# Performance work log

Hardware: AMD Instinct MI355X
Metric: run time of the kernel (lower is better)

Reference implementation:

```python
import jax, jax.numpy as jnp
import numpy as np

D, H, T, P1, P2, B = 1024, 16, 2048, 16, 16, 2
HD = D // H
EPS = 1e-6
NEG = -1e30


def _ln(x, g, b):
    mu = jnp.mean(x, axis=-1, keepdims=True)
    var = jnp.mean((x - mu) ** 2, axis=-1, keepdims=True)
    return (x - mu) * jax.lax.rsqrt(var + EPS) * g + b


def _split_heads(x):  # [B,S,D] -> [B,H,S,HD]
    b, s, _ = x.shape
    return x.reshape(b, s, H, HD).transpose(0, 2, 1, 3)


def _merge_heads(x):  # [B,H,S,HD] -> [B,S,D]
    b, _, s, _ = x.shape
    return x.transpose(0, 2, 1, 3).reshape(b, s, D)


def setup_inputs() -> dict:
    key = jax.random.key(0)
    ks = jax.random.split(key, 24)
    s = 0.02
    inp = {
        'x': jax.random.normal(ks[0], (B, T, D), jnp.float32),
        'p1': jax.random.normal(ks[1], (B, P1, D), jnp.float32),
        'p2': jax.random.normal(ks[2], (B, P2, D), jnp.float32),
        'prior_1': jax.random.uniform(ks[3], (B, T), jnp.float32),
        'prior_2': jax.random.uniform(ks[4], (B, T), jnp.float32),
        'mask': jnp.ones((B, T), jnp.float32),
        'Wq': s * jax.random.normal(ks[5], (D, D), jnp.float32),
        'bq': jnp.zeros((D,), jnp.float32),
        'Wk': s * jax.random.normal(ks[6], (D, D), jnp.float32),
        'bk': jnp.zeros((D,), jnp.float32),
        'Wv': s * jax.random.normal(ks[7], (D, D), jnp.float32),
        'bv': jnp.zeros((D,), jnp.float32),
        'ln2_g': jnp.ones((D,), jnp.float32),
        'ln2_b': jnp.zeros((D,), jnp.float32),
        'W1': s * jax.random.normal(ks[8], (D, D), jnp.float32),
        'b1': jnp.zeros((D,), jnp.float32),
        'W2': s * jax.random.normal(ks[9], (D, D), jnp.float32),
        'b2': jnp.zeros((D,), jnp.float32),
        'Wp1': s * jax.random.normal(ks[10], (D, D), jnp.float32),
        'bp1': jnp.zeros((D,), jnp.float32),
        'Wp2': s * jax.random.normal(ks[11], (D, D), jnp.float32),
        'bp2': jnp.zeros((D,), jnp.float32),
    }
    return inp


def reference(x, p1, p2, prior_1, prior_2, mask, Wq, bq, Wk, bk, Wv, bv,
              ln2_g, ln2_b, W1, b1, W2, b2, Wp1, bp1, Wp2, bp2):
    scale = 1.0 / jnp.sqrt(jnp.asarray(HD, x.dtype))
    # Q/K are [proj(x); p1; p2] (prompts enter unprojected), V only from x.
    q = _split_heads(jnp.concatenate([x @ Wq + bq, p1, p2], axis=1))
    k = _split_heads(jnp.concatenate([x @ Wk + bk, p1, p2], axis=1))
    v = _split_heads(x @ Wv + bv)
    scores = jnp.einsum('bhqd,bhkd->bhqk', q, k) * scale  # [B,H,T+P,T+P]

    word = scores[:, :, :T, :T]                                  # [B,H,T,T]
    p1s = jnp.swapaxes(scores[:, :, :T, T:T + P1], -1, -2)       # [B,H,P1,T]
    p2s = jnp.swapaxes(scores[:, :, :T, T + P1:], -1, -2)        # [B,H,P2,T]

    word = word + (1.0 - mask)[:, None, None, :] * NEG           # mask_logits
    wa = jax.nn.softmax(word, axis=-1)
    p1a = jax.nn.softmax(jax.nn.softmax(p1s, axis=-1) * prior_1[:, None, None, :], axis=-1)
    p2a = jax.nn.softmax(jax.nn.softmax(p2s, axis=-1) * prior_2[:, None, None, :], axis=-1)

    ctx = jnp.einsum('bhqk,bhkd->bhqd', wa, v)    # [B,H,T,HD]
    p1_v = jnp.einsum('bhpk,bhkd->bhpd', p1a, ctx)
    p2_v = jnp.einsum('bhpk,bhkd->bhpd', p2a, ctx)

    residual = x + _merge_heads(ctx)
    out = _ln(residual, ln2_g, ln2_b)
    out = jax.nn.gelu(out @ W1 + b1, approximate=False)
    out = out @ W2 + b2 + residual

    p1_out = _ln(_merge_heads(p1_v) + p1, ln2_g, ln2_b)
    p1_out = jax.nn.gelu(p1_out @ Wp1 + bp1, approximate=False)

    p2_out = _ln(_merge_heads(p2_v) + p2, ln2_g, ln2_b)
    p2_out = jax.nn.gelu(p2_out @ Wp2 + bp2, approximate=False)
    return (out, p1_out, p2_out)
```

## Files before the change

### kernel.cpp

```cpp
#include <hip/hip_runtime.h>

#define DEV __device__ __forceinline__

typedef unsigned short u16;
typedef unsigned int   u32;
typedef short  s16x8  __attribute__((ext_vector_type(8)));
typedef float  f32x4  __attribute__((ext_vector_type(4)));
typedef float  f32x16 __attribute__((ext_vector_type(16)));

constexpr int Bc = 2, Hc = 16, Tc = 2048, Dc = 1024, HDc = 64, Mc = 4096;
constexpr int TP = Tc + 32;
constexpr float SCALEc = 0.125f;
constexpr float LOG2E = 1.44269504088896340736f;
constexpr float SCALE2c = SCALEc * LOG2E;
constexpr float NEGc = -1e30f;

typedef __attribute__((address_space(3))) void lds_void;
typedef const __attribute__((address_space(1))) void g_void;

DEV void gload16(const void* g, void* l) {
  __builtin_amdgcn_global_load_lds((g_void*)g, (lds_void*)l, 16, 0, 0);
}

DEV int swz(int r) { return (r & 7) ^ ((r >> 3) & 7); }

DEV u32 bfr(float f) {
  u32 u = __float_as_uint(f);
  return (u + 0x7fffu + ((u >> 16) & 1u)) >> 16;
}
DEV u32 cvtpk(float a, float b) {
  u32 r;
  asm("v_cvt_pk_bf16_f32 %0, %1, %2" : "=v"(r) : "v"(a), "v"(b));
  return r;
}
DEV s16x8 mk8(u32 w0, u32 w1, u32 w2, u32 w3) {
  union { u32 u[4]; s16x8 v; } x;
  x.u[0] = w0; x.u[1] = w1; x.u[2] = w2; x.u[3] = w3;
  return x.v;
}
DEV float geluf(float x) { return 0.5f * x * (1.0f + erff(x * 0.70710678118654752440f)); }

DEV float wredS(float v) {
  #pragma unroll
  for (int o = 32; o; o >>= 1) v += __shfl_xor(v, o);
  return v;
}
DEV float wredM(float v) {
  #pragma unroll
  for (int o = 32; o; o >>= 1) v = fmaxf(v, __shfl_xor(v, o));
  return v;
}
DEV float bredS(float v, float* sm) {
  v = wredS(v);
  __syncthreads();
  if ((threadIdx.x & 63) == 0) sm[threadIdx.x >> 6] = v;
  __syncthreads();
  return sm[0] + sm[1] + sm[2] + sm[3];
}
DEV float bredM(float v, float* sm) {
  v = wredM(v);
  __syncthreads();
  if ((threadIdx.x & 63) == 0) sm[threadIdx.x >> 6] = v;
  __syncthreads();
  return fmaxf(fmaxf(sm[0], sm[1]), fmaxf(sm[2], sm[3]));
}

__global__ __launch_bounds__(256) void transpose_w5_k(
    const float* __restrict__ Wq, const float* __restrict__ Wk,
    const float* __restrict__ Wv, const float* __restrict__ W1,
    const float* __restrict__ W2, const float* __restrict__ x,
    u16* __restrict__ WQKVT, u16* __restrict__ W1T, u16* __restrict__ W2T,
    u16* __restrict__ XB) {
  int z = blockIdx.z;
  if (z == 5) {
    int base = (int)(blockIdx.y * 32 + blockIdx.x);
    int i0 = base * 1024 + (int)threadIdx.x;
    #pragma unroll
    for (int k = 0; k < 4; ++k) {
      int i = i0 + k * 256;
      float4 v = ((const float4*)x)[i];
      ushort4 u;
      u.x = (u16)bfr(v.x); u.y = (u16)bfr(v.y);
      u.z = (u16)bfr(v.z); u.w = (u16)bfr(v.w);
      ((ushort4*)XB)[i] = u;
    }
    return;
  }
  __shared__ float tile[32][33];
  int bx = blockIdx.x, by = blockIdx.y;
  const float* src = (z == 0) ? Wq : (z == 1) ? Wk : (z == 2) ? Wv
                    : (z == 3) ? W1 : W2;
  u16* dst = (z == 0) ? WQKVT
           : (z == 1) ? WQKVT + (size_t)1024 * 1024
           : (z == 2) ? WQKVT + (size_t)2 * 1024 * 1024
           : (z == 3) ? W1T : W2T;
  int tx = threadIdx.x & 31, ty = threadIdx.x >> 5;
  #pragma unroll
  for (int i = 0; i < 32; i += 8)
    tile[ty + i][tx] = src[(size_t)(by * 32 + ty + i) * Dc + bx * 32 + tx];
  __syncthreads();
  #pragma unroll
  for (int i = 0; i < 32; i += 8)
    dst[(size_t)(bx * 32 + ty + i) * Dc + by * 32 + tx] = (u16)bfr(tile[tx][ty + i]);
}

template <int MODE, int NBX, int NBY>
__global__ __launch_bounds__(256, 3) void gemm128_k(
    const u16* __restrict__ A, const u16* __restrict__ Bt,
    const float* __restrict__ bias0, const float* __restrict__ bias1,
    const float* __restrict__ bias2,
    u16* __restrict__ outQ, u16* __restrict__ outK, u16* __restrict__ outVT,
    u16* __restrict__ outB, float* __restrict__ outF,
    const float* __restrict__ resid) {
  __shared__ __align__(16) u16 smem[17408];
  u16* as0 = smem;
  u16* bs0 = smem + 2 * 128 * 32;
  const int tid = threadIdx.x, lane = tid & 63, wave = tid >> 6;
  const int wr = wave >> 1, wc = wave & 1;
  constexpr int RPX = NBX / 4, CPX = NBY / 2;
  const int bid = (int)blockIdx.x;
  const int xcd = bid & 7, l = bid >> 3;
  const int row0 = ((xcd & 3) * RPX + l % RPX) * 128;
  const int col0 = ((xcd >> 2) * CPX + l / RPX) * 128;

  f32x4 zero4;
  #pragma unroll
  for (int r = 0; r < 4; ++r) zero4[r] = 0.f;
  f32x4 acc[4][4];
  #pragma unroll
  for (int i = 0; i < 4; ++i)
    #pragma unroll
    for (int j = 0; j < 4; ++j) acc[i][j] = zero4;

  auto stage = [&](int buf, int kt) {
    const int k0 = kt * 32;
    #pragma unroll
    for (int is = 0; is < 2; ++is) {
      int q = is * 256 + tid; int r = q >> 2, c = q & 3, g = c ^ ((r >> 1) & 3);
      gload16(A + (size_t)(row0 + r) * Dc + k0 + g * 8,
              as0 + (size_t)buf * 4096 + (is * 256 + wave * 64) * 8);
    }
    #pragma unroll
    for (int is = 0; is < 2; ++is) {
      int q = is * 256 + tid; int r = q >> 2, c = q & 3, g = c ^ ((r >> 1) & 3);
      gload16(Bt + (size_t)(col0 + r) * Dc + k0 + g * 8,
              bs0 + (size_t)buf * 4096 + (is * 256 + wave * 64) * 8);
    }
  };

  stage(0, 0);
  asm volatile("s_waitcnt vmcnt(0)" ::: "memory");
  __syncthreads();

  int cur = 0;
  for (int kt = 0; kt < 32; ++kt) {
    if (kt + 1 < 32) stage(cur ^ 1, kt + 1);
    s16x8 af[4], bfv[4];
    #pragma unroll
    for (int f = 0; f < 4; ++f) {
      int r = wr * 64 + f * 16 + (lane & 15);
      int c = (lane >> 4) ^ ((r >> 1) & 3);
      af[f] = *(const s16x8*)&as0[cur * 4096 + r * 32 + c * 8];
    }
    #pragma unroll
    for (int f = 0; f < 4; ++f) {
      int r = wc * 64 + f * 16 + (lane & 15);
      int c = (lane >> 4) ^ ((r >> 1) & 3);
      bfv[f] = *(const s16x8*)&bs0[cur * 4096 + r * 32 + c * 8];
    }
    __builtin_amdgcn_s_setprio(1);
    #pragma unroll
    for (int i = 0; i < 4; ++i)
      #pragma unroll
      for (int j = 0; j < 4; ++j)
        acc[i][j] = __builtin_amdgcn_mfma_f32_16x16x32_bf16(af[i], bfv[j], acc[i][j], 0, 0, 0);
    __builtin_amdgcn_s_setprio(0);
    __syncthreads();
    cur ^= 1;
  }

  if (MODE == 0) {
    const int which = col0 >> 10;
    const float* bias = (which == 0) ? bias0 : (which == 1) ? bias1 : bias2;
    if (which == 2) {
      const int CSV = 129;
      u16* ct = smem;
      #pragma unroll
      for (int i = 0; i < 4; ++i)
        #pragma unroll
        for (int j = 0; j < 4; ++j)
          #pragma unroll
          for (int r = 0; r < 4; ++r) {
            int rl = wr * 64 + i * 16 + (lane >> 4) * 4 + r;
            int cl = wc * 64 + j * 16 + (lane & 15);
            float v = acc[i][j][r] + bias[(col0 + cl) & 1023];
            ct[rl * CSV + cl] = (u16)bfr(v);
          }
      __syncthreads();
      int bb = row0 >> 11, tbase = row0 & 2047;
      #pragma unroll
      for (int it = 0; it < 16; ++it) {
        int linear = it * 256 + tid;
        int dcol = linear >> 5, q4 = linear & 31;
        int t = q4 * 4;
        int n = (col0 & 1023) + dcol;
        int hh = n >> 6, dd = n & 63;
        ushort4 val;
        val.x = ct[(t + 0) * CSV + dcol];
        val.y = ct[(t + 1) * CSV + dcol];
        val.z = ct[(t + 2) * CSV + dcol];
        val.w = ct[(t + 3) * CSV + dcol];
        *(ushort4*)&outVT[((size_t)(bb * Hc + hh) * 64 + dd) * Tc + tbase + t] = val;
      }
    } else {
      const int CS = 136;
      u16* ct = smem;
      #pragma unroll
      for (int i = 0; i < 4; ++i)
        #pragma unroll
        for (int j = 0; j < 4; ++j)
          #pragma unroll
          for (int r = 0; r < 4; ++r) {
            int rl = wr * 64 + i * 16 + (lane >> 4) * 4 + r;
            int cl = wc * 64 + j * 16 + (lane & 15);
            float v = acc[i][j][r] + bias[(col0 + cl) & 1023];
            ct[rl * CS + cl] = (u16)bfr(v);
          }
      __syncthreads();
      #pragma unroll
      for (int it = 0; it < 16; ++it) {
        int linear = it * 256 + tid;
        int row = linear >> 5, c4 = (linear & 31) * 4;
        ushort4 val = *(const ushort4*)&ct[row * CS + c4];
        int grow = row0 + row;
        int col = col0 + c4;
        int n = col & 1023;
        int hh = n >> 6, d = n & 63, bb = grow >> 11, t = grow & 2047;
        if (which == 0)
          *(ushort4*)&outQ[(((size_t)(bb * Hc + hh) * Tc + t) << 6) + d] = val;
        else
          *(ushort4*)&outK[(((size_t)(bb * Hc + hh) * TP + t) << 6) + d] = val;
      }
    }
  } else if (MODE == 1) {
    const int CS = 136;
    u16* ct = smem;
    #pragma unroll
    for (int i = 0; i < 4; ++i)
      #pragma unroll
      for (int j = 0; j < 4; ++j)
        #pragma unroll
        for (int r = 0; r < 4; ++r) {
          int rl = wr * 64 + i * 16 + (lane >> 4) * 4 + r;
          int cl = wc * 64 + j * 16 + (lane & 15);
          float v = geluf(acc[i][j][r] + bias0[col0 + cl]);
          ct[rl * CS + cl] = (u16)bfr(v);
        }
    __syncthreads();
    #pragma unroll
    for (int it = 0; it < 16; ++it) {
      int linear = it * 256 + tid;
      int row = linear >> 5, c4 = (linear & 31) * 4;
      ushort4 val = *(const ushort4*)&ct[row * CS + c4];
      *(ushort4*)&outB[(size_t)(row0 + row) * Dc + col0 + c4] = val;
    }
  } else {
    const int CSF = 132;
    float* cf = (float*)smem;
    #pragma unroll
    for (int p = 0; p < 2; ++p) {
      if (wr == p) {
        #pragma unroll
        for (int i = 0; i < 4; ++i)
          #pragma unroll
          for (int j = 0; j < 4; ++j)
            #pragma unroll
            for (int r = 0; r < 4; ++r) {
              int rl = i * 16 + (lane >> 4) * 4 + r;
              int cl = wc * 64 + j * 16 + (lane & 15);
              cf[rl * CSF + cl] = acc[i][j][r];
            }
      }
      __syncthreads();
      #pragma unroll
      for (int it = 0; it < 8; ++it) {
        int linear = it * 256 + tid;
        int row = linear >> 5, c4 = (linear & 31) * 4;
        float4 v = *(const float4*)&cf[row * CSF + c4];
        int grow = row0 + p * 64 + row;
        int col = col0 + c4;
        float4 rr = *(const float4*)&resid[(size_t)grow * Dc + col];
        float4 o;
        o.x = v.x + bias0[col + 0] + rr.x;
        o.y = v.y + bias0[col + 1] + rr.y;
        o.z = v.z + bias0[col + 2] + rr.z;
        o.w = v.w + bias0[col + 3] + rr.w;
        *(float4*)&outF[(size_t)grow * Dc + col] = o;
      }
      __syncthreads();
    }
  }
}

__global__ __launch_bounds__(256, 2) void attn_k(
    const u16* __restrict__ qb,
    const u16* __restrict__ kb,
    const u16* __restrict__ vt,
    const float* __restrict__ maskp,
    const float* __restrict__ p1, const float* __restrict__ p2,
    float* __restrict__ OP0, float* __restrict__ OP1,
    float* __restrict__ ML,
    float* __restrict__ SP) {
  __shared__ __align__(16) u16 kls[2][64 * 64];
  __shared__ __align__(16) u16 vls[2][64 * 64];
  __shared__ __align__(16) u16 kpls[32 * 64];
  __shared__ float mls[1024];

  const int tid = threadIdx.x, lane = tid & 63, wave = tid >> 6;
  const int wg = ((int)blockIdx.x & 7) * 128 + ((int)blockIdx.x >> 3);
  const int ks = wg & 1, qt = (wg >> 1) & 15, bh = wg >> 5;
  const int b = bh >> 4;
  const int lo = lane & 31, h5 = lane >> 5;
  const size_t kbase = (size_t)bh * TP * 64;
  const size_t vbase = (size_t)bh * 64 * Tc;

  for (int i = tid; i < 1024; i += 256)
    mls[i] = (1.0f - maskp[(size_t)b * Tc + ks * 1024 + i]) * NEGc;

  if (ks == 0) {
    int r = tid >> 3, cg = tid & 7, g = cg ^ swz(r);
    int h = bh & 15;
    const float* src = (r < 16)
        ? (p1 + (size_t)(b * 16 + r) * Dc + h * 64 + g * 8)
        : (p2 + (size_t)(b * 16 + (r - 16)) * Dc + h * 64 + g * 8);
    float4 a = *(const float4*)src;
    float4 c = *(const float4*)(src + 4);
    *(s16x8*)&kpls[tid * 8] = mk8(cvtpk(a.x, a.y), cvtpk(a.z, a.w),
                                  cvtpk(c.x, c.y), cvtpk(c.z, c.w));
  }

  const int q0 = qt * 128 + wave * 32;
  s16x8 qf[4];
  #pragma unroll
  for (int kc = 0; kc < 4; ++kc)
    qf[kc] = *(const s16x8*)(qb + ((size_t)bh * Tc + q0 + lo) * 64 + kc * 16 + h5 * 8);

  auto stageKV = [&](int buf, int kt2) {
    #pragma unroll
    for (int is = 0; is < 2; ++is) {
      int q = is * 256 + tid; int r = q >> 3, c = q & 7, g = c ^ swz(r);
      gload16(kb + kbase + (size_t)(kt2 * 64 + r) * 64 + g * 8,
              &kls[buf][(is * 256 + wave * 64) * 8]);
      gload16(vt + vbase + (size_t)r * Tc + kt2 * 64 + g * 8,
              &vls[buf][(is * 256 + wave * 64) * 8]);
    }
  };

  stageKV(0, ks * 16);
  asm volatile("s_waitcnt vmcnt(0)" ::: "memory");
  __syncthreads();

  f32x16 zero16;
  #pragma unroll
  for (int r = 0; r < 16; ++r) zero16[r] = 0.f;
  f32x16 O0 = zero16, O1 = zero16, racc = zero16;

  int cur = 0;
  for (int kt = 0; kt < 16; ++kt) {
    if (kt + 1 < 16) stageKV(cur ^ 1, ks * 16 + kt + 1);

    #pragma unroll
    for (int c = 0; c < 2; ++c) {
      f32x16 s = zero16;
      __builtin_amdgcn_s_setprio(1);
      #pragma unroll
      for (int kc = 0; kc < 4; ++kc) {
        int r = c * 32 + lo;
        int ci = (kc * 2 + h5) ^ swz(r);
        s16x8 kf = *(const s16x8*)&kls[cur][r * 64 + ci * 8];
        s = __builtin_amdgcn_mfma_f32_32x32x16_bf16(kf, qf[kc], s, 0, 0, 0);
      }
      __builtin_amdgcn_s_setprio(0);

      float4 mq[4];
      #pragma unroll
      for (int g = 0; g < 4; ++g)
        mq[g] = *(const float4*)&mls[kt * 64 + c * 32 + 4 * h5 + 8 * g];

      float p[16];
      #pragma unroll
      for (int r = 0; r < 16; ++r) {
        float mv = (&mq[r >> 2].x)[r & 3];
        p[r] = exp2f(s[r] * SCALE2c + mv);
        racc[r] += p[r];
      }

      #pragma unroll
      for (int k1 = 0; k1 < 2; ++k1) {
        u32 w0 = cvtpk(p[8 * k1 + 0], p[8 * k1 + 1]);
        u32 w1 = cvtpk(p[8 * k1 + 2], p[8 * k1 + 3]);
        u32 w2 = cvtpk(p[8 * k1 + 4], p[8 * k1 + 5]);
        u32 w3 = cvtpk(p[8 * k1 + 6], p[8 * k1 + 7]);
        asm volatile("v_permlane32_swap_b32 %0, %1" : "+v"(w2), "+v"(w0));
        asm volatile("v_permlane32_swap_b32 %0, %1" : "+v"(w3), "+v"(w1));
        s16x8 pf = mk8(w0, w1, w2, w3);
        __builtin_amdgcn_s_setprio(1);
        #pragma unroll
        for (int db = 0; db < 2; ++db) {
          int d = db * 32 + lo;
          int ci = (c * 4 + k1 * 2 + h5) ^ swz(d);
          s16x8 vf = *(const s16x8*)&vls[cur][d * 64 + ci * 8];
          if (db == 0) O0 = __builtin_amdgcn_mfma_f32_32x32x16_bf16(pf, vf, O0, 0, 0, 0);
          else         O1 = __builtin_amdgcn_mfma_f32_32x32x16_bf16(pf, vf, O1, 0, 0, 0);
        }
        __builtin_amdgcn_s_setprio(0);
      }
    }
    __syncthreads();
    cur ^= 1;
  }

  if (ks == 0) {
    f32x16 sp = zero16;
    #pragma unroll
    for (int kc = 0; kc < 4; ++kc) {
      int ci = (kc * 2 + h5) ^ swz(lo);
      s16x8 kf = *(const s16x8*)&kpls[lo * 64 + ci * 8];
      sp = __builtin_amdgcn_mfma_f32_32x32x16_bf16(kf, qf[kc], sp, 0, 0, 0);
    }
    #pragma unroll
    for (int r = 0; r < 16; ++r) {
      int pr = (r & 3) + 8 * (r >> 2) + 4 * h5;
      SP[((size_t)bh * 32 + pr) * Tc + q0 + lo] = sp[r] * SCALEc;
    }
  }

  float* dst = ks ? OP1 : OP0;
  #pragma unroll
  for (int r = 0; r < 16; ++r) {
    int row = q0 + (r & 3) + 8 * (r >> 2) + 4 * h5;
    dst[((size_t)bh * Tc + row) * 64 + lo]      = O0[r];
    dst[((size_t)bh * Tc + row) * 64 + 32 + lo] = O1[r];
  }
  float lt = 0.f;
  #pragma unroll
  for (int r = 0; r < 16; ++r) lt += racc[r];
  lt += __shfl_xor(lt, 32);
  if (lane < 32)
    ML[((size_t)ks * 32 + bh) * Tc + q0 + lo] = lt;
}

__global__ __launch_bounds__(256) void prompt_softmax_k(float* __restrict__ SP,
                                                        const float* __restrict__ pr1,
                                                        const float* __restrict__ pr2) {
  __shared__ float sm[4];
  int row = blockIdx.x;
  int bh = row >> 5, p = row & 31, b = bh >> 4;
  const float* prior = (p < 16 ? pr1 : pr2) + (size_t)b * Tc;
  float* s = SP + (size_t)row * Tc;
  int tid = threadIdx.x;
  float v[8], pw[8];
  #pragma unroll
  for (int i = 0; i < 8; ++i) { int t = tid + i * 256; v[i] = s[t]; pw[i] = prior[t]; }
  float mx = -INFINITY;
  #pragma unroll
  for (int i = 0; i < 8; ++i) mx = fmaxf(mx, v[i]);
  mx = bredM(mx, sm);
  float sum = 0.f;
  #pragma unroll
  for (int i = 0; i < 8; ++i) { v[i] = __expf(v[i] - mx); sum += v[i]; }
  sum = bredS(sum, sm);
  float inv = 1.0f / sum;
  float mx2 = -INFINITY;
  #pragma unroll
  for (int i = 0; i < 8; ++i) { v[i] = v[i] * inv * pw[i]; mx2 = fmaxf(mx2, v[i]); }
  mx2 = bredM(mx2, sm);
  float sum2 = 0.f;
  #pragma unroll
  for (int i = 0; i < 8; ++i) { v[i] = __expf(v[i] - mx2); sum2 += v[i]; }
  sum2 = bredS(sum2, sm);
  float inv2 = 1.0f / sum2;
  #pragma unroll
  for (int i = 0; i < 8; ++i) s[tid + i * 256] = v[i] * inv2;
}

__global__ __launch_bounds__(256) void pv_partial_k(const float* __restrict__ PA,
                                                    float* __restrict__ ctx,
                                                    const float* __restrict__ OP1,
                                                    const float* __restrict__ ML,
                                                    float* __restrict__ PVP) {
  __shared__ float pal[32][128];
  __shared__ float lsm[128];
  const int bh = blockIdx.x, ts = blockIdx.y;
  const int tid = threadIdx.x;
  const int t0 = ts * 128;
  const float* pabase = PA + (size_t)bh * 32 * Tc;

  if (tid < 128) {
    size_t r = (size_t)bh * Tc + t0 + tid;
    lsm[tid] = 1.0f / (ML[r] + ML[(size_t)32 * Tc + r]);
  }
  __syncthreads();
  #pragma unroll
  for (int pp = 0; pp < 8; ++pp) {
    int idx = pp * 256 + tid;
    int rr = idx >> 4, c4 = (idx & 15) * 4;
    size_t row = (size_t)bh * Tc + t0 + rr;
    float4 v0 = *(const float4*)(ctx + row * 64 + c4);
    float4 v1 = *(const float4*)(OP1 + row * 64 + c4);
    float li = lsm[rr];
    float4 o;
    o.x = (v0.x + v1.x) * li;
    o.y = (v0.y + v1.y) * li;
    o.z = (v0.z + v1.z) * li;
    o.w = (v0.w + v1.w) * li;
    *(float4*)(ctx + row * 64 + c4) = o;
  }
  __syncthreads();

  #pragma unroll
  for (int i = 0; i < 4; ++i) {
    int e = tid + i * 256;
    int p = e >> 5, c4 = e & 31;
    *(float4*)&pal[p][c4 * 4] = *(const float4*)&pabase[(size_t)p * Tc + t0 + c4 * 4];
  }
  __syncthreads();

  const int d4 = tid & 15, p0 = tid >> 4;
  const float* cb = ctx + ((size_t)bh * Tc + t0) * 64 + d4 * 4;
  float4 a0 = make_float4(0.f, 0.f, 0.f, 0.f);
  float4 a1 = make_float4(0.f, 0.f, 0.f, 0.f);
  for (int tt = 0; tt < 128; ++tt) {
    float4 v = *(const float4*)(cb + (size_t)tt * 64);
    float w0 = pal[p0][tt], w1 = pal[p0 + 16][tt];
    a0.x += w0 * v.x; a0.y += w0 * v.y; a0.z += w0 * v.z; a0.w += w0 * v.w;
    a1.x += w1 * v.x; a1.y += w1 * v.y; a1.z += w1 * v.z; a1.w += w1 * v.w;
  }
  float* o = PVP + (((size_t)ts * 32 + bh) * 32) * 64 + d4 * 4;
  *(float4*)(o + (size_t)p0 * 64) = a0;
  *(float4*)(o + (size_t)(p0 + 16) * 64) = a1;
}

__global__ __launch_bounds__(256) void resln_k(const float* __restrict__ x,
                                               const float* __restrict__ ctx,
                                               const float* __restrict__ g,
                                               const float* __restrict__ be,
                                               float* __restrict__ res,
                                               u16* __restrict__ lnout) {
  __shared__ float sm[4];
  int row = blockIdx.x;
  int b = row >> 11, t = row & 2047;
  int tid = threadIdx.x, c4 = tid * 4;
  int h = c4 >> 6, d = c4 & 63;
  float4 xv = *(const float4*)(x + (size_t)row * Dc + c4);
  float4 cv = *(const float4*)(ctx + (((size_t)(b * Hc + h) * Tc + t) << 6) + d);
  float r0 = xv.x + cv.x, r1 = xv.y + cv.y, r2 = xv.z + cv.z, r3 = xv.w + cv.w;
  float4 rr; rr.x = r0; rr.y = r1; rr.z = r2; rr.w = r3;
  *(float4*)(res + (size_t)row * Dc + c4) = rr;
  float s = bredS(r0 + r1 + r2 + r3, sm);
  float sq = bredS(r0 * r0 + r1 * r1 + r2 * r2 + r3 * r3, sm);
  float mu = s * (1.0f / Dc);
  float var = sq * (1.0f / Dc) - mu * mu;
  float rs = rsqrtf(var + 1e-6f);
  ushort4 o;
  o.x = (u16)bfr((r0 - mu) * rs * g[c4 + 0] + be[c4 + 0]);
  o.y = (u16)bfr((r1 - mu) * rs * g[c4 + 1] + be[c4 + 1]);
  o.z = (u16)bfr((r2 - mu) * rs * g[c4 + 2] + be[c4 + 2]);
  o.w = (u16)bfr((r3 - mu) * rs * g[c4 + 3] + be[c4 + 3]);
  *(ushort4*)(lnout + (size_t)row * Dc + c4) = o;
}

__global__ __launch_bounds__(256) void promptln_k(const float* __restrict__ PVP,
                                                  const float* __restrict__ p1,
                                                  const float* __restrict__ p2,
                                                  const float* __restrict__ g,
                                                  const float* __restrict__ be,
                                                  float* __restrict__ PMLN) {
  __shared__ float sm[4];
  int row = blockIdx.x;
  int b = row >> 5, j = row & 31;
  int tid = threadIdx.x, c4 = tid * 4;
  int h = c4 >> 6, d = c4 & 63;
  int bh = b * Hc + h;
  const float* pr = (j < 16) ? (p1 + (size_t)(b * 16 + j) * Dc + c4)
                             : (p2 + (size_t)(b * 16 + j - 16) * Dc + c4);
  float4 pv4 = make_float4(0.f, 0.f, 0.f, 0.f);
  #pragma unroll
  for (int ts = 0; ts < 16; ++ts) {
    float4 v = *(const float4*)(PVP + (((size_t)ts * 32 + bh) * 32 + j) * 64 + d);
    pv4.x += v.x; pv4.y += v.y; pv4.z += v.z; pv4.w += v.w;
  }
  float4 pp4 = *(const float4*)pr;
  float r0 = pv4.x + pp4.x, r1 = pv4.y + pp4.y, r2 = pv4.z + pp4.z, r3 = pv4.w + pp4.w;
  float s = bredS(r0 + r1 + r2 + r3, sm);
  float sq = bredS(r0 * r0 + r1 * r1 + r2 * r2 + r3 * r3, sm);
  float mu = s * (1.0f / Dc);
  float var = sq * (1.0f / Dc) - mu * mu;
  float rs = rsqrtf(var + 1e-6f);
  float4 o;
  o.x = (r0 - mu) * rs * g[c4 + 0] + be[c4 + 0];
  o.y = (r1 - mu) * rs * g[c4 + 1] + be[c4 + 1];
  o.z = (r2 - mu) * rs * g[c4 + 2] + be[c4 + 2];
  o.w = (r3 - mu) * rs * g[c4 + 3] + be[c4 + 3];
  *(float4*)(PMLN + (size_t)row * Dc + c4) = o;
}

__global__ __launch_bounds__(256) void pffn_partial_k(const float* __restrict__ PMLN,
                                                      const float* __restrict__ Wp1,
                                                      const float* __restrict__ Wp2,
                                                      float* __restrict__ PB) {
  __shared__ float pm[32][32];
  const int tid = threadIdx.x;
  const int ks = blockIdx.x, ct = blockIdx.y, s = blockIdx.z;
  const int c = ct * 256 + tid;
  const int k0 = ks * 32;
  const float* W = s ? Wp2 : Wp1;

  #pragma unroll
  for (int i = 0; i < 4; ++i) {
    int e = tid + i * 256;
    int r = e >> 5, kk = e & 31;
    int grow = (r >> 4) * 32 + s * 16 + (r & 15);
    pm[r][kk] = PMLN[(size_t)grow * Dc + k0 + kk];
  }
  __syncthreads();

  float acc[32];
  #pragma unroll
  for (int r = 0; r < 32; ++r) acc[r] = 0.f;
  for (int kk = 0; kk < 32; ++kk) {
    float w = W[(size_t)(k0 + kk) * Dc + c];
    #pragma unroll
    for (int r = 0; r < 32; ++r) acc[r] += pm[r][kk] * w;
  }

  float* pb = PB + (((size_t)ks * 2 + s) * 32) * Dc + c;
  #pragma unroll
  for (int r = 0; r < 32; ++r) pb[(size_t)r * Dc] = acc[r];
}

__global__ __launch_bounds__(256) void pffn_reduce_k(const float* __restrict__ PB,
                                                     const float* __restrict__ bp1,
                                                     const float* __restrict__ bp2,
                                                     float* __restrict__ out) {
  int e = blockIdx.x * 256 + threadIdx.x;
  int s = e >> 15, rem = e & 32767;
  int r = rem >> 10, c = rem & 1023;
  float sum = 0.f;
  const float* pb = PB + ((size_t)s * 32 + r) * Dc + c;
  #pragma unroll
  for (int ks = 0; ks < 32; ++ks) sum += pb[(size_t)ks * 2 * 32 * Dc];
  const float* bp = s ? bp2 : bp1;
  out[(size_t)Mc * Dc + (size_t)s * (32 * Dc) + (size_t)r * Dc + c] = geluf(sum + bp[c]);
}

extern "C" void kernel_launch(void* const* d_in, const int* in_sizes, int n_in,
                              void* d_out, int out_size, void* d_ws, size_t ws_size,
                              hipStream_t stream) {
  (void)in_sizes; (void)n_in; (void)out_size; (void)ws_size;
  const float* x   = (const float*)d_in[0];
  const float* p1  = (const float*)d_in[1];
  const float* p2  = (const float*)d_in[2];
  const float* pr1 = (const float*)d_in[3];
  const float* pr2 = (const float*)d_in[4];
  const float* msk = (const float*)d_in[5];
  const float* Wq  = (const float*)d_in[6];
  const float* bq  = (const float*)d_in[7];
  const float* Wk  = (const float*)d_in[8];
  const float* bk  = (const float*)d_in[9];
  const float* Wv  = (const float*)d_in[10];
  const float* bv  = (const float*)d_in[11];
  const float* g2  = (const float*)d_in[12];
  const float* be2 = (const float*)d_in[13];
  const float* W1  = (const float*)d_in[14];
  const float* b1  = (const float*)d_in[15];
  const float* W2  = (const float*)d_in[16];
  const float* b2  = (const float*)d_in[17];
  const float* Wp1 = (const float*)d_in[18];
  const float* bp1 = (const float*)d_in[19];
  const float* Wp2 = (const float*)d_in[20];
  const float* bp2 = (const float*)d_in[21];

  char* ws = (char*)d_ws;
  size_t off = 0;
  auto alloc = [&](size_t bytes) {
    void* p = ws + off;
    off += (bytes + 255) & ~(size_t)255;
    return p;
  };
  u16* WQKVT = (u16*)alloc((size_t)3072 * 1024 * 2);
  u16* W1T   = (u16*)alloc((size_t)1024 * 1024 * 2);
  u16* W2T   = (u16*)alloc((size_t)1024 * 1024 * 2);
  u16* XB    = (u16*)alloc((size_t)Mc * Dc * 2);
  u16* QB    = (u16*)alloc((size_t)32 * Tc * 64 * 2);
  u16* KB    = (u16*)alloc((size_t)32 * TP * 64 * 2);
  u16* H1    = (u16*)alloc((size_t)Mc * Dc * 2);
  u16* VT    = (u16*)alloc((size_t)32 * 64 * Tc * 2);
  float* CTX = (float*)alloc((size_t)32 * Tc * 64 * 4);
  float* SP  = (float*)alloc((size_t)32 * 32 * Tc * 4);
  float* RES = (float*)alloc((size_t)Mc * Dc * 4);
  float* PMLN = (float*)alloc((size_t)64 * Dc * 4);
  float* ML  = (float*)alloc((size_t)2 * 32 * Tc * 4);
  float* PVP = (float*)alloc((size_t)16 * 32 * 32 * 64 * 4);
  u16* LNOUT = XB;
  float* PB  = SP;
  float* OP0 = CTX;
  float* OP1 = RES;

  float* outMain = (float*)d_out;

  transpose_w5_k<<<dim3(32, 32, 6), 256, 0, stream>>>(Wq, Wk, Wv, W1, W2, x,
                                                      WQKVT, W1T, W2T, XB);
  gemm128_k<0, 32, 24><<<768, 256, 0, stream>>>(XB, WQKVT, bq, bk, bv, QB, KB,
                                                VT, nullptr, nullptr, nullptr);
  attn_k<<<1024, 256, 0, stream>>>(QB, KB, VT, msk, p1, p2, OP0, OP1, ML, SP);
  prompt_softmax_k<<<1024, 256, 0, stream>>>(SP, pr1, pr2);
  pv_partial_k<<<dim3(32, 16), 256, 0, stream>>>(SP, OP0, OP1, ML, PVP);
  resln_k<<<4096, 256, 0, stream>>>(x, CTX, g2, be2, RES, LNOUT);
  promptln_k<<<64, 256, 0, stream>>>(PVP, p1, p2, g2, be2, PMLN);
  pffn_partial_k<<<dim3(32, 4, 2), 256, 0, stream>>>(PMLN, Wp1, Wp2, PB);
  pffn_reduce_k<<<256, 256, 0, stream>>>(PB, bp1, bp2, outMain);
  gemm128_k<1, 32, 8><<<256, 256, 0, stream>>>(LNOUT, W1T, b1, nullptr, nullptr,
                                               nullptr, nullptr, nullptr, H1,
                                               nullptr, nullptr);
  gemm128_k<2, 32, 8><<<256, 256, 0, stream>>>(H1, W2T, b2, nullptr, nullptr,
                                               nullptr, nullptr, nullptr, nullptr,
                                               outMain, RES);
}
```

Baseline: 211.7 us.

## Store attention partial outputs as bf16 and widen the transpose tiles

```diff
diff --git a/kernel.cpp b/kernel.cpp
--- a/kernel.cpp
+++ b/kernel.cpp
@@ -28,6 +28,7 @@
   u32 u = __float_as_uint(f);
   return (u + 0x7fffu + ((u >> 16) & 1u)) >> 16;
 }
+DEV float b2f(u32 lo16) { return __uint_as_float(lo16 << 16); }
 DEV u32 cvtpk(float a, float b) {
   u32 r;
   asm("v_cvt_pk_bf16_f32 %0, %1, %2" : "=v"(r) : "v"(a), "v"(b));
@@ -73,10 +74,10 @@
     u16* __restrict__ XB) {
   int z = blockIdx.z;
   if (z == 5) {
-    int base = (int)(blockIdx.y * 32 + blockIdx.x);
-    int i0 = base * 1024 + (int)threadIdx.x;
-    #pragma unroll
-    for (int k = 0; k < 4; ++k) {
+    int base = (int)(blockIdx.y * 16 + blockIdx.x);
+    int i0 = base * 4096 + (int)threadIdx.x;
+    #pragma unroll
+    for (int k = 0; k < 16; ++k) {
       int i = i0 + k * 256;
       float4 v = ((const float4*)x)[i];
       ushort4 u;
@@ -86,7 +87,7 @@
     }
     return;
   }
-  __shared__ float tile[32][33];
+  __shared__ float tile[64][65];
   int bx = blockIdx.x, by = blockIdx.y;
   const float* src = (z == 0) ? Wq : (z == 1) ? Wk : (z == 2) ? Wv
                     : (z == 3) ? W1 : W2;
@@ -94,14 +95,22 @@
            : (z == 1) ? WQKVT + (size_t)1024 * 1024
            : (z == 2) ? WQKVT + (size_t)2 * 1024 * 1024
            : (z == 3) ? W1T : W2T;
-  int tx = threadIdx.x & 31, ty = threadIdx.x >> 5;
-  #pragma unroll
-  for (int i = 0; i < 32; i += 8)
-    tile[ty + i][tx] = src[(size_t)(by * 32 + ty + i) * Dc + bx * 32 + tx];
-  __syncthreads();
-  #pragma unroll
-  for (int i = 0; i < 32; i += 8)
-    dst[(size_t)(bx * 32 + ty + i) * Dc + by * 32 + tx] = (u16)bfr(tile[tx][ty + i]);
+  int tx = threadIdx.x & 63, ty = threadIdx.x >> 6;
+  #pragma unroll
+  for (int i = 0; i < 64; i += 4)
+    tile[ty + i][tx] = src[(size_t)(by * 64 + ty + i) * Dc + bx * 64 + tx];
+  __syncthreads();
+  int quad = threadIdx.x & 15, rw0 = threadIdx.x >> 4;
+  #pragma unroll
+  for (int it = 0; it < 4; ++it) {
+    int rw = it * 16 + rw0;
+    ushort4 u;
+    u.x = (u16)bfr(tile[quad * 4 + 0][rw]);
+    u.y = (u16)bfr(tile[quad * 4 + 1][rw]);
+    u.z = (u16)bfr(tile[quad * 4 + 2][rw]);
+    u.w = (u16)bfr(tile[quad * 4 + 3][rw]);
+    *(ushort4*)&dst[(size_t)(bx * 64 + rw) * Dc + by * 64 + quad * 4] = u;
+  }
 }
 
 template <int MODE, int NBX, int NBY>
@@ -308,7 +317,7 @@
     const u16* __restrict__ vt,
     const float* __restrict__ maskp,
     const float* __restrict__ p1, const float* __restrict__ p2,
-    float* __restrict__ OP0, float* __restrict__ OP1,
+    u16* __restrict__ OP0B, u16* __restrict__ OP1B,
     float* __restrict__ ML,
     float* __restrict__ SP) {
   __shared__ __align__(16) u16 kls[2][64 * 64];
@@ -435,12 +444,17 @@
     }
   }
 
-  float* dst = ks ? OP1 : OP0;
+  u32* dstw = (u32*)(ks ? OP1B : OP0B);
   #pragma unroll
   for (int r = 0; r < 16; ++r) {
     int row = q0 + (r & 3) + 8 * (r >> 2) + 4 * h5;
-    dst[((size_t)bh * Tc + row) * 64 + lo]      = O0[r];
-    dst[((size_t)bh * Tc + row) * 64 + 32 + lo] = O1[r];
+    int srcE = (h5 << 5) | ((2 * lo) & 31);
+    int srcO = (h5 << 5) | ((2 * lo + 1) & 31);
+    float aE = __shfl(O0[r], srcE), bE = __shfl(O1[r], srcE);
+    float aO = __shfl(O0[r], srcO), bO = __shfl(O1[r], srcO);
+    float vE = (lo < 16) ? aE : bE;
+    float vO = (lo < 16) ? aO : bO;
+    dstw[((size_t)bh * Tc + row) * 32 + lo] = cvtpk(vE, vO);
   }
   float lt = 0.f;
   #pragma unroll
@@ -485,9 +499,10 @@
 }
 
 __global__ __launch_bounds__(256) void pv_partial_k(const float* __restrict__ PA,
+                                                    const u16* __restrict__ OP0B,
+                                                    const u16* __restrict__ OP1B,
+                                                    const float* __restrict__ ML,
                                                     float* __restrict__ ctx,
-                                                    const float* __restrict__ OP1,
-                                                    const float* __restrict__ ML,
                                                     float* __restrict__ PVP) {
   __shared__ float pal[32][128];
   __shared__ float lsm[128];
@@ -495,6 +510,8 @@
   const int tid = threadIdx.x;
   const int t0 = ts * 128;
   const float* pabase = PA + (size_t)bh * 32 * Tc;
+  const u32* w0p = (const u32*)OP0B;
+  const u32* w1p = (const u32*)OP1B;
 
   if (tid < 128) {
     size_t r = (size_t)bh * Tc + t0 + tid;
@@ -505,16 +522,16 @@
   for (int pp = 0; pp < 8; ++pp) {
     int idx = pp * 256 + tid;
     int rr = idx >> 4, c4 = (idx & 15) * 4;
-    size_t row = (size_t)bh * Tc + t0 + rr;
-    float4 v0 = *(const float4*)(ctx + row * 64 + c4);
-    float4 v1 = *(const float4*)(OP1 + row * 64 + c4);
+    size_t rowb = ((size_t)bh * Tc + t0 + rr) * 32 + (c4 >> 1);
+    u32 a0 = w0p[rowb], a1 = w0p[rowb + 1];
+    u32 b0 = w1p[rowb], b1 = w1p[rowb + 1];
     float li = lsm[rr];
     float4 o;
-    o.x = (v0.x + v1.x) * li;
-    o.y = (v0.y + v1.y) * li;
-    o.z = (v0.z + v1.z) * li;
-    o.w = (v0.w + v1.w) * li;
-    *(float4*)(ctx + row * 64 + c4) = o;
+    o.x = (b2f(a0 & 0xffffu) + b2f(b0 & 0xffffu)) * li;
+    o.y = (b2f(a0 >> 16)     + b2f(b0 >> 16))     * li;
+    o.z = (b2f(a1 & 0xffffu) + b2f(b1 & 0xffffu)) * li;
+    o.w = (b2f(a1 >> 16)     + b2f(b1 >> 16))     * li;
+    *(float4*)(ctx + ((size_t)bh * Tc + t0 + rr) * 64 + c4) = o;
   }
   __syncthreads();
 
@@ -704,18 +721,18 @@
   float* PVP = (float*)alloc((size_t)16 * 32 * 32 * 64 * 4);
   u16* LNOUT = XB;
   float* PB  = SP;
-  float* OP0 = CTX;
-  float* OP1 = RES;
+  u16* OP0B  = (u16*)RES;
+  u16* OP1B  = (u16*)RES + (size_t)32 * Tc * 64;
 
   float* outMain = (float*)d_out;
 
-  transpose_w5_k<<<dim3(32, 32, 6), 256, 0, stream>>>(Wq, Wk, Wv, W1, W2, x,
+  transpose_w5_k<<<dim3(16, 16, 6), 256, 0, stream>>>(Wq, Wk, Wv, W1, W2, x,
                                                       WQKVT, W1T, W2T, XB);
   gemm128_k<0, 32, 24><<<768, 256, 0, stream>>>(XB, WQKVT, bq, bk, bv, QB, KB,
                                                 VT, nullptr, nullptr, nullptr);
-  attn_k<<<1024, 256, 0, stream>>>(QB, KB, VT, msk, p1, p2, OP0, OP1, ML, SP);
+  attn_k<<<1024, 256, 0, stream>>>(QB, KB, VT, msk, p1, p2, OP0B, OP1B, ML, SP);
   prompt_softmax_k<<<1024, 256, 0, stream>>>(SP, pr1, pr2);
-  pv_partial_k<<<dim3(32, 16), 256, 0, stream>>>(SP, OP0, OP1, ML, PVP);
+  pv_partial_k<<<dim3(32, 16), 256, 0, stream>>>(SP, OP0B, OP1B, ML, CTX, PVP);
   resln_k<<<4096, 256, 0, stream>>>(x, CTX, g2, be2, RES, LNOUT);
   promptln_k<<<64, 256, 0, stream>>>(PVP, p1, p2, g2, be2, PMLN);
   pffn_partial_k<<<dim3(32, 4, 2), 256, 0, stream>>>(PMLN, Wp1, Wp2, PB);
```

New measurement: 211.0 us. No clear change (-0.3%).
